# Performance work log

Measured on AMD Instinct MI355X. Metric: run time of the kernel, lower is better.

The kernel has to match this reference:

```python
import jax, jax.numpy as jnp
import numpy as np

B = 32768      # batch
N_IN = 128     # input nodes
L = 8          # topological layers
W = 256        # nodes per layer
K = 16         # fan-in per node


def setup_inputs() -> dict:
    key = jax.random.key(0)
    k_x, k_w, k_b, k_e = jax.random.split(key, 4)
    inputs = jax.random.normal(k_x, (B, N_IN), dtype=jnp.float32)
    # scale weights down so sigmoid isn't saturated with fan-in 16
    weights = jax.random.normal(k_w, (L, W, K), dtype=jnp.float32) * 0.25
    biases = jax.random.normal(k_b, (L, W), dtype=jnp.float32) * 0.1
    # DAG-valid edges: layer l may only gather from the N_IN + l*W already-computed nodes
    ek = jax.random.split(k_e, L)
    edge_idx = jnp.stack([
        jax.random.randint(ek[l], (W, K), 0, N_IN + l * W, dtype=jnp.int32)
        for l in range(L)
    ])  # [L, W, K]
    return {"inputs": inputs, "weights": weights, "biases": biases,
            "edge_idx": edge_idx}


def reference(inputs, weights, biases, edge_idx):
    # values buffer starts as the input-node activations: [B, N_IN]
    vals = inputs
    n_layers = weights.shape[0]
    for l in range(n_layers):
        gathered = vals[:, edge_idx[l]]                      # [B, W, K] per-node gather
        pre = jnp.einsum('bwk,wk->bw', gathered, weights[l]) + biases[l]
        vals = jnp.concatenate([vals, jax.nn.sigmoid(pre)], axis=1)
    # output nodes are the last layer, concatenated in order
    return vals[:, -W:]
```

## Files before the change

### kernel.cpp

```cpp
#include <hip/hip_runtime.h>
#include <hip/hip_bf16.h>
#include <hip/hip_fp16.h>


#define NB   32768
#define NIN  128
#define NL   8
#define NW   256
#define NK   16
#define RPB  16
#define STORED (NIN + (NL - 1) * NW)
#define NPARAM (NL * NW * NK)

typedef __fp16 fp16v2 __attribute__((ext_vector_type(2)));

__device__ __forceinline__ unsigned pk16(float a, float b) {
    fp16v2 p = __builtin_amdgcn_cvt_pkrtz(a, b);
    return __builtin_bit_cast(unsigned, p);
}

__device__ __forceinline__ __half2 as_h2(unsigned u) {
    return __builtin_bit_cast(__half2, u);
}

__device__ __forceinline__ float fast_sigmoid(float x) {
    return __builtin_amdgcn_rcpf(1.0f + __expf(-x));
}

__device__ __forceinline__ void fma_feat(__half2 acc[4], __half2 w2, uint4 p) {
    acc[0] = __hfma2(as_h2(p.x), w2, acc[0]);
    acc[1] = __hfma2(as_h2(p.y), w2, acc[1]);
    acc[2] = __hfma2(as_h2(p.z), w2, acc[2]);
    acc[3] = __hfma2(as_h2(p.w), w2, acc[3]);
}

template <bool PRE>
__global__ __launch_bounds__(256, 2)
void ffn_gather_kernel(const float* __restrict__ inputs,
                       const float* __restrict__ weights,
                       const float* __restrict__ biases,
                       const int*   __restrict__ edge_idx,
                       const int*   __restrict__ idxb,
                       const unsigned* __restrict__ wpk,
                       float* __restrict__ out)
{
    __shared__ uint4 valsA[STORED];
    __shared__ uint4 valsB[STORED];

    const int t = threadIdx.x;
    const long long row0 = (long long)blockIdx.x * RPB;
    const char* vbaseA = (const char*)valsA;
    const char* vbaseB = (const char*)valsB;

    {
        const int f = t & 127;
        const long long r0 = row0 + ((t >> 7) << 3);
        float v[8];
        #pragma unroll
        for (int r = 0; r < 8; ++r) v[r] = inputs[(r0 + r) * NIN + f];
        uint4 p;
        p.x = pk16(v[0], v[1]);
        p.y = pk16(v[2], v[3]);
        p.z = pk16(v[4], v[5]);
        p.w = pk16(v[6], v[7]);
        if (t < NIN) valsA[f] = p; else valsB[f] = p;
    }
    __syncthreads();

    #pragma unroll
    for (int l = 0; l < NL; ++l) {
        const int base = (l * NW + t) * NK;

        const float b = biases[l * NW + t];
        __half2 accA[4], accB[4];
        const __half2 bb = __float2half2_rn(b);
        #pragma unroll
        for (int j = 0; j < 4; ++j) { accA[j] = bb; accB[j] = bb; }

        #pragma unroll
        for (int kk = 0; kk < NK / 4; ++kk) {
            int4 o4;
            __half2 w0, w1, w2, w3;
            if (PRE) {
                o4 = ((const int4*)(idxb + base))[kk];
                uint4 wp = ((const uint4*)(wpk + base))[kk];
                w0 = as_h2(wp.x); w1 = as_h2(wp.y);
                w2 = as_h2(wp.z); w3 = as_h2(wp.w);
            } else {
                int4 i4 = ((const int4*)(edge_idx + base))[kk];
                o4.x = i4.x << 4; o4.y = i4.y << 4;
                o4.z = i4.z << 4; o4.w = i4.w << 4;
                float4 w4 = ((const float4*)(weights + base))[kk];
                w0 = __float2half2_rn(w4.x);
                w1 = __float2half2_rn(w4.y);
                w2 = __float2half2_rn(w4.z);
                w3 = __float2half2_rn(w4.w);
            }
            const uint4 a0 = *(const uint4*)(vbaseA + o4.x);
            const uint4 b0 = *(const uint4*)(vbaseB + o4.x);
            const uint4 a1 = *(const uint4*)(vbaseA + o4.y);
            const uint4 b1 = *(const uint4*)(vbaseB + o4.y);
            const uint4 a2 = *(const uint4*)(vbaseA + o4.z);
            const uint4 b2 = *(const uint4*)(vbaseB + o4.z);
            const uint4 a3 = *(const uint4*)(vbaseA + o4.w);
            const uint4 b3 = *(const uint4*)(vbaseB + o4.w);
            fma_feat(accA, w0, a0);
            fma_feat(accB, w0, b0);
            fma_feat(accA, w1, a1);
            fma_feat(accB, w1, b1);
            fma_feat(accA, w2, a2);
            fma_feat(accB, w2, b2);
            fma_feat(accA, w3, a3);
            fma_feat(accB, w3, b3);
        }

        float sA[8], sB[8];
        #pragma unroll
        for (int j = 0; j < 4; ++j) {
            sA[2 * j + 0] = fast_sigmoid(__low2float(accA[j]));
            sA[2 * j + 1] = fast_sigmoid(__high2float(accA[j]));
            sB[2 * j + 0] = fast_sigmoid(__low2float(accB[j]));
            sB[2 * j + 1] = fast_sigmoid(__high2float(accB[j]));
        }

        if (l < NL - 1) {
            uint4 pA, pB;
            pA.x = pk16(sA[0], sA[1]); pA.y = pk16(sA[2], sA[3]);
            pA.z = pk16(sA[4], sA[5]); pA.w = pk16(sA[6], sA[7]);
            pB.x = pk16(sB[0], sB[1]); pB.y = pk16(sB[2], sB[3]);
            pB.z = pk16(sB[4], sB[5]); pB.w = pk16(sB[6], sB[7]);
            valsA[NIN + l * NW + t] = pA;
            valsB[NIN + l * NW + t] = pB;
            __syncthreads();
        } else {
            #pragma unroll
            for (int r = 0; r < 8; ++r) {
                out[(row0 + r) * NW + t]     = sA[r];
                out[(row0 + 8 + r) * NW + t] = sB[r];
            }
        }
    }
}

__global__ __launch_bounds__(256)
void balance_prepass_kernel(const float* __restrict__ weights,
                            const int* __restrict__ edge_idx,
                            int* __restrict__ idxb,
                            unsigned* __restrict__ wpk)
{
    const int t = blockIdx.x * 256 + threadIdx.x;
    const int lane = threadIdx.x & 63;
    const int base = t * NK;

    int   idxv[NK];
    float wv[NK];
    #pragma unroll
    for (int j = 0; j < NK; ++j) {
        idxv[j] = edge_idx[base + j];
        wv[j]   = weights[base + j];
    }

    unsigned long long cntp = 0;
    #pragma unroll
    for (int j = 0; j < NK; ++j)
        cntp += 1ull << ((idxv[j] & 7) * 8);

    unsigned long long x = cntp;
    x += x << 8;
    x += x << 16;
    x += x << 32;
    unsigned long long cur = x << 8;

    const int rot = (2 * (lane & 7) + ((lane >> 3) & 7)) & 15;
    #pragma unroll
    for (int j = 0; j < NK; ++j) {
        const int g   = idxv[j] & 7;
        const int pos = (int)((cur >> (g * 8)) & 0xFF);
        cur += 1ull << (g * 8);
        const int slot = (pos + rot) & 15;
        idxb[base + slot] = idxv[j] << 4;
        wpk [base + slot] = pk16(wv[j], wv[j]);
    }
}

extern "C" void kernel_launch(void* const* d_in, const int* in_sizes, int n_in,
                              void* d_out, int out_size, void* d_ws, size_t ws_size,
                              hipStream_t stream)
{
    const float* inputs   = (const float*)d_in[0];
    const float* weights  = (const float*)d_in[1];
    const float* biases   = (const float*)d_in[2];
    const int*   edge_idx = (const int*)d_in[3];
    float* out = (float*)d_out;

    dim3 grid(NB / RPB);
    dim3 block(NW);

    const size_t need = (size_t)NPARAM * 4 * 2;
    if (ws_size >= need) {
        int*      idxb = (int*)d_ws;
        unsigned* wpk  = (unsigned*)((char*)d_ws + (size_t)NPARAM * 4);
        balance_prepass_kernel<<<NL * NW / 256, 256, 0, stream>>>(
            weights, edge_idx, idxb, wpk);
        ffn_gather_kernel<true><<<grid, block, 0, stream>>>(
            inputs, weights, biases, edge_idx, idxb, wpk, out);
    } else {
        ffn_gather_kernel<false><<<grid, block, 0, stream>>>(
            inputs, weights, biases, edge_idx, nullptr, nullptr, out);
    }
}
```

Before: 134.1 us.

## Halve rows per block and duplicate LDS values with offset copy for bank balancing

Result: slower. 149.7 us (+11.7%).

```diff
diff --git a/kernel.cpp b/kernel.cpp
--- a/kernel.cpp
+++ b/kernel.cpp
@@ -8,11 +8,14 @@
 #define NL   8
 #define NW   256
 #define NK   16
-#define RPB  16
+#define RPB  8
 #define STORED (NIN + (NL - 1) * NW)
 #define NPARAM (NL * NW * NK)
+#define C1OFF  (STORED * 16)
+#define LDSBYTES (C1OFF + 16 + STORED * 16)
 
 typedef __fp16 fp16v2 __attribute__((ext_vector_type(2)));
+typedef unsigned long long u64;
 
 __device__ __forceinline__ unsigned pk16(float a, float b) {
     fp16v2 p = __builtin_amdgcn_cvt_pkrtz(a, b);
@@ -44,26 +47,22 @@
                        const unsigned* __restrict__ wpk,
                        float* __restrict__ out)
 {
-    __shared__ uint4 valsA[STORED];
-    __shared__ uint4 valsB[STORED];
+    __shared__ __align__(16) char vals[LDSBYTES];
 
     const int t = threadIdx.x;
     const long long row0 = (long long)blockIdx.x * RPB;
-    const char* vbaseA = (const char*)valsA;
-    const char* vbaseB = (const char*)valsB;
 
     {
         const int f = t & 127;
-        const long long r0 = row0 + ((t >> 7) << 3);
         float v[8];
         #pragma unroll
-        for (int r = 0; r < 8; ++r) v[r] = inputs[(r0 + r) * NIN + f];
+        for (int r = 0; r < 8; ++r) v[r] = inputs[(row0 + r) * NIN + f];
         uint4 p;
         p.x = pk16(v[0], v[1]);
         p.y = pk16(v[2], v[3]);
         p.z = pk16(v[4], v[5]);
         p.w = pk16(v[6], v[7]);
-        if (t < NIN) valsA[f] = p; else valsB[f] = p;
+        *(uint4*)(vals + ((t >> 7) ? (C1OFF + 16 + f * 16) : (f * 16))) = p;
     }
     __syncthreads();
 
@@ -72,10 +71,10 @@
         const int base = (l * NW + t) * NK;
 
         const float b = biases[l * NW + t];
-        __half2 accA[4], accB[4];
+        __half2 acc[4];
         const __half2 bb = __float2half2_rn(b);
         #pragma unroll
-        for (int j = 0; j < 4; ++j) { accA[j] = bb; accB[j] = bb; }
+        for (int j = 0; j < 4; ++j) acc[j] = bb;
 
         #pragma unroll
         for (int kk = 0; kk < NK / 4; ++kk) {
@@ -96,48 +95,35 @@
                 w2 = __float2half2_rn(w4.z);
                 w3 = __float2half2_rn(w4.w);
             }
-            const uint4 a0 = *(const uint4*)(vbaseA + o4.x);
-            const uint4 b0 = *(const uint4*)(vbaseB + o4.x);
-            const uint4 a1 = *(const uint4*)(vbaseA + o4.y);
-            const uint4 b1 = *(const uint4*)(vbaseB + o4.y);
-            const uint4 a2 = *(const uint4*)(vbaseA + o4.z);
-            const uint4 b2 = *(const uint4*)(vbaseB + o4.z);
-            const uint4 a3 = *(const uint4*)(vbaseA + o4.w);
-            const uint4 b3 = *(const uint4*)(vbaseB + o4.w);
-            fma_feat(accA, w0, a0);
-            fma_feat(accB, w0, b0);
-            fma_feat(accA, w1, a1);
-            fma_feat(accB, w1, b1);
-            fma_feat(accA, w2, a2);
-            fma_feat(accB, w2, b2);
-            fma_feat(accA, w3, a3);
-            fma_feat(accB, w3, b3);
-        }
-
-        float sA[8], sB[8];
+            const uint4 a0 = *(const uint4*)(vals + o4.x);
+            const uint4 a1 = *(const uint4*)(vals + o4.y);
+            const uint4 a2 = *(const uint4*)(vals + o4.z);
+            const uint4 a3 = *(const uint4*)(vals + o4.w);
+            fma_feat(acc, w0, a0);
+            fma_feat(acc, w1, a1);
+            fma_feat(acc, w2, a2);
+            fma_feat(acc, w3, a3);
+        }
+
+        float s[8];
         #pragma unroll
         for (int j = 0; j < 4; ++j) {
-            sA[2 * j + 0] = fast_sigmoid(__low2float(accA[j]));
-            sA[2 * j + 1] = fast_sigmoid(__high2float(accA[j]));
-            sB[2 * j + 0] = fast_sigmoid(__low2float(accB[j]));
-            sB[2 * j + 1] = fast_sigmoid(__high2float(accB[j]));
+            s[2 * j + 0] = fast_sigmoid(__low2float(acc[j]));
+            s[2 * j + 1] = fast_sigmoid(__high2float(acc[j]));
         }
 
         if (l < NL - 1) {
-            uint4 pA, pB;
-            pA.x = pk16(sA[0], sA[1]); pA.y = pk16(sA[2], sA[3]);
-            pA.z = pk16(sA[4], sA[5]); pA.w = pk16(sA[6], sA[7]);
-            pB.x = pk16(sB[0], sB[1]); pB.y = pk16(sB[2], sB[3]);
-            pB.z = pk16(sB[4], sB[5]); pB.w = pk16(sB[6], sB[7]);
-            valsA[NIN + l * NW + t] = pA;
-            valsB[NIN + l * NW + t] = pB;
+            uint4 p;
+            p.x = pk16(s[0], s[1]); p.y = pk16(s[2], s[3]);
+            p.z = pk16(s[4], s[5]); p.w = pk16(s[6], s[7]);
+            const int F = NIN + l * NW + t;
+            *(uint4*)(vals + F * 16) = p;
+            *(uint4*)(vals + C1OFF + 16 + F * 16) = p;
             __syncthreads();
         } else {
             #pragma unroll
-            for (int r = 0; r < 8; ++r) {
-                out[(row0 + r) * NW + t]     = sA[r];
-                out[(row0 + 8 + r) * NW + t] = sB[r];
-            }
+            for (int r = 0; r < 8; ++r)
+                out[(row0 + r) * NW + t] = s[r];
         }
     }
 }
@@ -149,7 +135,7 @@
                             unsigned* __restrict__ wpk)
 {
     const int t = blockIdx.x * 256 + threadIdx.x;
-    const int lane = threadIdx.x & 63;
+    const int lane = t & 63;
     const int base = t * NK;
 
     int   idxv[NK];
@@ -160,25 +146,58 @@
         wv[j]   = weights[base + j];
     }
 
-    unsigned long long cntp = 0;
+    u64 cntp = 0;
     #pragma unroll
     for (int j = 0; j < NK; ++j)
         cntp += 1ull << ((idxv[j] & 7) * 8);
 
-    unsigned long long x = cntp;
+    u64 s_pk = 0;
+    #pragma unroll
+    for (int it = 0; it < 3; ++it) {
+        #pragma unroll
+        for (int g = 0; g < 8; ++g) {
+            const int gp = (g + 7) & 7;
+            int sp = (int)((s_pk >> (gp * 8)) & 0xFF);
+            int c  = (int)((cntp >> (g * 8)) & 0xFF);
+            int v  = sp + c - 2;
+            v = v < 0 ? 0 : (v > c ? c : v);
+            s_pk = (s_pk & ~(0xFFull << (g * 8))) | ((u64)v << (g * 8));
+        }
+    }
+    const u64 keep_pk = cntp - s_pk;
+
+    u64 used = 0;
+    int fg[NK], sh[NK];
+    #pragma unroll
+    for (int j = 0; j < NK; ++j) {
+        const int g  = idxv[j] & 7;
+        const int u_ = (int)((used >> (g * 8)) & 0xFF);
+        used += 1ull << (g * 8);
+        const int kp = (int)((keep_pk >> (g * 8)) & 0xFF);
+        sh[j] = (u_ >= kp) ? 1 : 0;
+        fg[j] = (g + sh[j]) & 7;
+    }
+
+    u64 fcnt = 0;
+    #pragma unroll
+    for (int j = 0; j < NK; ++j)
+        fcnt += 1ull << (fg[j] * 8);
+
+    u64 x = fcnt;
     x += x << 8;
     x += x << 16;
     x += x << 32;
-    unsigned long long cur = x << 8;
+    u64 cur = x << 8;
 
     const int rot = (2 * (lane & 7) + ((lane >> 3) & 7)) & 15;
     #pragma unroll
     for (int j = 0; j < NK; ++j) {
-        const int g   = idxv[j] & 7;
+        const int g   = fg[j];
         const int pos = (int)((cur >> (g * 8)) & 0xFF);
         cur += 1ull << (g * 8);
         const int slot = (pos + rot) & 15;
-        idxb[base + slot] = idxv[j] << 4;
+        idxb[base + slot] = sh[j] ? (C1OFF + 16 + (idxv[j] << 4))
+                                  : (idxv[j] << 4);
         wpk [base + slot] = pk16(wv[j], wv[j]);
     }
 }
```

## Permute node-to-thread mapping per layer to reduce LDS bank conflicts

Applied to the files above, without the earlier changes.

New measurement: 146.2 us. +9.1%, slower.

```diff
diff --git a/kernel.cpp b/kernel.cpp
--- a/kernel.cpp
+++ b/kernel.cpp
@@ -13,6 +13,7 @@
 #define NPARAM (NL * NW * NK)
 
 typedef __fp16 fp16v2 __attribute__((ext_vector_type(2)));
+typedef unsigned long long u64;
 
 __device__ __forceinline__ unsigned pk16(float a, float b) {
     fp16v2 p = __builtin_amdgcn_cvt_pkrtz(a, b);
@@ -34,7 +35,7 @@
     acc[3] = __hfma2(as_h2(p.w), w2, acc[3]);
 }
 
-template <bool PRE>
+template <bool PRE, bool PERM>
 __global__ __launch_bounds__(256, 2)
 void ffn_gather_kernel(const float* __restrict__ inputs,
                        const float* __restrict__ weights,
@@ -42,6 +43,7 @@
                        const int*   __restrict__ edge_idx,
                        const int*   __restrict__ idxb,
                        const unsigned* __restrict__ wpk,
+                       const int*   __restrict__ punit,
                        float* __restrict__ out)
 {
     __shared__ uint4 valsA[STORED];
@@ -71,7 +73,8 @@
     for (int l = 0; l < NL; ++l) {
         const int base = (l * NW + t) * NK;
 
-        const float b = biases[l * NW + t];
+        const int u = PERM ? punit[l * NW + t] : t;
+        const float b = biases[l * NW + u];
         __half2 accA[4], accB[4];
         const __half2 bb = __float2half2_rn(b);
         #pragma unroll
@@ -135,41 +138,90 @@
         } else {
             #pragma unroll
             for (int r = 0; r < 8; ++r) {
-                out[(row0 + r) * NW + t]     = sA[r];
-                out[(row0 + 8 + r) * NW + t] = sB[r];
+                out[(row0 + r) * NW + u]     = sA[r];
+                out[(row0 + 8 + r) * NW + u] = sB[r];
             }
         }
     }
 }
 
 __global__ __launch_bounds__(256)
-void balance_prepass_kernel(const float* __restrict__ weights,
-                            const int* __restrict__ edge_idx,
-                            int* __restrict__ idxb,
-                            unsigned* __restrict__ wpk)
-{
-    const int t = blockIdx.x * 256 + threadIdx.x;
-    const int lane = threadIdx.x & 63;
-    const int base = t * NK;
+void partition_kernel(const int* __restrict__ edge_idx,
+                      int* __restrict__ t_of,
+                      int* __restrict__ punit)
+{
+    __shared__ int keys[NW];
+    const int l = blockIdx.x;
+    const int u = threadIdx.x;
+
+    u64 c = 0;
+    #pragma unroll
+    for (int j = 0; j < NK; ++j)
+        c += 1ull << ((edge_idx[(l * NW + u) * NK + j] & 7) * 8);
+
+    int best_g = 0, best_v = -1;
+    #pragma unroll
+    for (int g = 0; g < 8; ++g) {
+        const int v = (int)((c >> (g * 8)) & 0xFF);
+        if (v > best_v) { best_v = v; best_g = g; }
+    }
+    keys[u] = best_g * NW + u;
+    __syncthreads();
+
+    const int r = u & 7;
+    const int myk = keys[u];
+    int rank = 0;
+    #pragma unroll
+    for (int j = 0; j < 32; ++j)
+        rank += (keys[8 * j + r] < myk) ? 1 : 0;
+
+    const int o = (rank + 4 * r) & 31;
+    const int t = o * 8 + r;
+    t_of[l * NW + u]  = t;
+    punit[l * NW + t] = u;
+}
+
+template <bool PERM>
+__global__ __launch_bounds__(256)
+void emit_kernel(const float* __restrict__ weights,
+                 const int* __restrict__ edge_idx,
+                 const int* __restrict__ t_of,
+                 const int* __restrict__ punit,
+                 int* __restrict__ idxb,
+                 unsigned* __restrict__ wpk)
+{
+    const int l = blockIdx.x;
+    const int t = threadIdx.x;
+    const int u = PERM ? punit[l * NW + t] : t;
+    const int srcbase = (l * NW + u) * NK;
+    const int dstbase = (l * NW + t) * NK;
+    const int lane = t & 63;
 
     int   idxv[NK];
     float wv[NK];
     #pragma unroll
     for (int j = 0; j < NK; ++j) {
-        idxv[j] = edge_idx[base + j];
-        wv[j]   = weights[base + j];
-    }
-
-    unsigned long long cntp = 0;
+        int ix = edge_idx[srcbase + j];
+        if (PERM && ix >= NIN) {
+            const int f  = ix - NIN;
+            const int ls = f >> 8;
+            const int us = f & 255;
+            ix = NIN + (ls << 8) + t_of[ls * NW + us];
+        }
+        idxv[j] = ix;
+        wv[j]   = weights[srcbase + j];
+    }
+
+    u64 cntp = 0;
     #pragma unroll
     for (int j = 0; j < NK; ++j)
         cntp += 1ull << ((idxv[j] & 7) * 8);
 
-    unsigned long long x = cntp;
+    u64 x = cntp;
     x += x << 8;
     x += x << 16;
     x += x << 32;
-    unsigned long long cur = x << 8;
+    u64 cur = x << 8;
 
     const int rot = (2 * (lane & 7) + ((lane >> 3) & 7)) & 15;
     #pragma unroll
@@ -178,8 +230,8 @@
         const int pos = (int)((cur >> (g * 8)) & 0xFF);
         cur += 1ull << (g * 8);
         const int slot = (pos + rot) & 15;
-        idxb[base + slot] = idxv[j] << 4;
-        wpk [base + slot] = pk16(wv[j], wv[j]);
+        idxb[dstbase + slot] = idxv[j] << 4;
+        wpk [dstbase + slot] = pk16(wv[j], wv[j]);
     }
 }
 
@@ -196,16 +248,31 @@
     dim3 grid(NB / RPB);
     dim3 block(NW);
 
-    const size_t need = (size_t)NPARAM * 4 * 2;
-    if (ws_size >= need) {
+    const size_t sz_idxb  = (size_t)NPARAM * 4;
+    const size_t sz_wpk   = (size_t)NPARAM * 4;
+    const size_t sz_map   = (size_t)NL * NW * 4;
+    const size_t need_basic = sz_idxb + sz_wpk;
+    const size_t need_full  = need_basic + 2 * sz_map;
+
+    if (ws_size >= need_full) {
+        int*      idxb  = (int*)d_ws;
+        unsigned* wpk   = (unsigned*)((char*)d_ws + sz_idxb);
+        int*      t_of  = (int*)((char*)d_ws + need_basic);
+        int*      punit = (int*)((char*)d_ws + need_basic + sz_map);
+        partition_kernel<<<NL, NW, 0, stream>>>(edge_idx, t_of, punit);
+        emit_kernel<true><<<NL, NW, 0, stream>>>(weights, edge_idx,
+                                                 t_of, punit, idxb, wpk);
+        ffn_gather_kernel<true, true><<<grid, block, 0, stream>>>(
+            inputs, weights, biases, edge_idx, idxb, wpk, punit, out);
+    } else if (ws_size >= need_basic) {
         int*      idxb = (int*)d_ws;
-        unsigned* wpk  = (unsigned*)((char*)d_ws + (size_t)NPARAM * 4);
-        balance_prepass_kernel<<<NL * NW / 256, 256, 0, stream>>>(
-            weights, edge_idx, idxb, wpk);
-        ffn_gather_kernel<true><<<grid, block, 0, stream>>>(
-            inputs, weights, biases, edge_idx, idxb, wpk, out);
+        unsigned* wpk  = (unsigned*)((char*)d_ws + sz_idxb);
+        emit_kernel<false><<<NL, NW, 0, stream>>>(weights, edge_idx,
+                                                  nullptr, nullptr, idxb, wpk);
+        ffn_gather_kernel<true, false><<<grid, block, 0, stream>>>(
+            inputs, weights, biases, edge_idx, idxb, wpk, nullptr, out);
     } else {
-        ffn_gather_kernel<false><<<grid, block, 0, stream>>>(
-            inputs, weights, biases, edge_idx, nullptr, nullptr, out);
-    }
-}
+        ffn_gather_kernel<false, false><<<grid, block, 0, stream>>>(
+            inputs, weights, biases, edge_idx, nullptr, nullptr, nullptr, out);
+    }
+}
```

## Pre-pack inputs to fp16 in global memory and gather layer 0 from it

Applied to the files above, without the earlier changes.

Result: slower. 144.1 us (+7.5%).

```diff
diff --git a/kernel.cpp b/kernel.cpp
--- a/kernel.cpp
+++ b/kernel.cpp
@@ -11,8 +11,10 @@
 #define RPB  16
 #define STORED (NIN + (NL - 1) * NW)
 #define NPARAM (NL * NW * NK)
+#define NOCT (NB / 8)
 
 typedef __fp16 fp16v2 __attribute__((ext_vector_type(2)));
+typedef unsigned long long u64;
 
 __device__ __forceinline__ unsigned pk16(float a, float b) {
     fp16v2 p = __builtin_amdgcn_cvt_pkrtz(a, b);
@@ -34,7 +36,7 @@
     acc[3] = __hfma2(as_h2(p.w), w2, acc[3]);
 }
 
-template <bool PRE>
+template <bool PRE, bool G0>
 __global__ __launch_bounds__(256, 2)
 void ffn_gather_kernel(const float* __restrict__ inputs,
                        const float* __restrict__ weights,
@@ -42,6 +44,7 @@
                        const int*   __restrict__ edge_idx,
                        const int*   __restrict__ idxb,
                        const unsigned* __restrict__ wpk,
+                       const uint4* __restrict__ gin,
                        float* __restrict__ out)
 {
     __shared__ uint4 valsA[STORED];
@@ -65,10 +68,63 @@
         p.w = pk16(v[6], v[7]);
         if (t < NIN) valsA[f] = p; else valsB[f] = p;
     }
-    __syncthreads();
-
-    #pragma unroll
-    for (int l = 0; l < NL; ++l) {
+
+    if constexpr (G0) {
+        const char* gA = (const char*)(gin + (size_t)(2 * blockIdx.x)     * NIN);
+        const char* gB = (const char*)(gin + (size_t)(2 * blockIdx.x + 1) * NIN);
+        const int base = t * NK;
+        const float b = biases[t];
+        __half2 accA[4], accB[4];
+        const __half2 bb = __float2half2_rn(b);
+        #pragma unroll
+        for (int j = 0; j < 4; ++j) { accA[j] = bb; accB[j] = bb; }
+
+        #pragma unroll
+        for (int kk = 0; kk < NK / 4; ++kk) {
+            const int4 o4 = ((const int4*)(idxb + base))[kk];
+            const uint4 wp = ((const uint4*)(wpk + base))[kk];
+            const __half2 w0 = as_h2(wp.x), w1 = as_h2(wp.y);
+            const __half2 w2 = as_h2(wp.z), w3 = as_h2(wp.w);
+            const uint4 a0 = *(const uint4*)(gA + o4.x);
+            const uint4 b0 = *(const uint4*)(gB + o4.x);
+            const uint4 a1 = *(const uint4*)(gA + o4.y);
+            const uint4 b1 = *(const uint4*)(gB + o4.y);
+            const uint4 a2 = *(const uint4*)(gA + o4.z);
+            const uint4 b2 = *(const uint4*)(gB + o4.z);
+            const uint4 a3 = *(const uint4*)(gA + o4.w);
+            const uint4 b3 = *(const uint4*)(gB + o4.w);
+            fma_feat(accA, w0, a0);
+            fma_feat(accB, w0, b0);
+            fma_feat(accA, w1, a1);
+            fma_feat(accB, w1, b1);
+            fma_feat(accA, w2, a2);
+            fma_feat(accB, w2, b2);
+            fma_feat(accA, w3, a3);
+            fma_feat(accB, w3, b3);
+        }
+
+        float sA[8], sB[8];
+        #pragma unroll
+        for (int j = 0; j < 4; ++j) {
+            sA[2 * j + 0] = fast_sigmoid(__low2float(accA[j]));
+            sA[2 * j + 1] = fast_sigmoid(__high2float(accA[j]));
+            sB[2 * j + 0] = fast_sigmoid(__low2float(accB[j]));
+            sB[2 * j + 1] = fast_sigmoid(__high2float(accB[j]));
+        }
+        uint4 pA, pB;
+        pA.x = pk16(sA[0], sA[1]); pA.y = pk16(sA[2], sA[3]);
+        pA.z = pk16(sA[4], sA[5]); pA.w = pk16(sA[6], sA[7]);
+        pB.x = pk16(sB[0], sB[1]); pB.y = pk16(sB[2], sB[3]);
+        pB.z = pk16(sB[4], sB[5]); pB.w = pk16(sB[6], sB[7]);
+        valsA[NIN + t] = pA;
+        valsB[NIN + t] = pB;
+        __syncthreads();
+    } else {
+        __syncthreads();
+    }
+
+    #pragma unroll
+    for (int l = G0 ? 1 : 0; l < NL; ++l) {
         const int base = (l * NW + t) * NK;
 
         const float b = biases[l * NW + t];
@@ -143,14 +199,33 @@
 }
 
 __global__ __launch_bounds__(256)
-void balance_prepass_kernel(const float* __restrict__ weights,
-                            const int* __restrict__ edge_idx,
-                            int* __restrict__ idxb,
-                            unsigned* __restrict__ wpk)
+void pack_inputs_kernel(const float* __restrict__ inputs,
+                        uint4* __restrict__ gin)
 {
-    const int t = blockIdx.x * 256 + threadIdx.x;
-    const int lane = threadIdx.x & 63;
-    const int base = t * NK;
+    const int tid = blockIdx.x * 256 + threadIdx.x;
+    const int oc = tid >> 7;
+    const int f  = tid & 127;
+    float v[8];
+    #pragma unroll
+    for (int r = 0; r < 8; ++r)
+        v[r] = inputs[(size_t)(oc * 8 + r) * NIN + f];
+    uint4 p;
+    p.x = pk16(v[0], v[1]);
+    p.y = pk16(v[2], v[3]);
+    p.z = pk16(v[4], v[5]);
+    p.w = pk16(v[6], v[7]);
+    gin[(size_t)oc * NIN + f] = p;
+}
+
+__global__ __launch_bounds__(256)
+void emit_kernel(const float* __restrict__ weights,
+                 const int* __restrict__ edge_idx,
+                 int* __restrict__ idxb,
+                 unsigned* __restrict__ wpk)
+{
+    const int tgid = blockIdx.x * 256 + threadIdx.x;
+    const int lane = tgid & 63;
+    const int base = tgid * NK;
 
     int   idxv[NK];
     float wv[NK];
@@ -160,23 +235,26 @@
         wv[j]   = weights[base + j];
     }
 
-    unsigned long long cntp = 0;
-    #pragma unroll
-    for (int j = 0; j < NK; ++j)
-        cntp += 1ull << ((idxv[j] & 7) * 8);
-
-    unsigned long long x = cntp;
-    x += x << 8;
-    x += x << 16;
-    x += x << 32;
-    unsigned long long cur = x << 8;
+    u64 cA = 0, cB = 0;
+    #pragma unroll
+    for (int j = 0; j < NK; ++j) {
+        const int g = idxv[j] & 15;
+        const u64 inc = 1ull << ((g & 7) * 8);
+        if (g < 8) cA += inc; else cB += inc;
+    }
+    u64 xA = cA; xA += xA << 8; xA += xA << 16; xA += xA << 32;
+    u64 xB = cB; xB += xB << 8; xB += xB << 16; xB += xB << 32;
+    const int totA = (int)((xA >> 56) & 0xFF);
+    u64 curA = xA << 8, curB = xB << 8;
 
     const int rot = (2 * (lane & 7) + ((lane >> 3) & 7)) & 15;
     #pragma unroll
     for (int j = 0; j < NK; ++j) {
-        const int g   = idxv[j] & 7;
-        const int pos = (int)((cur >> (g * 8)) & 0xFF);
-        cur += 1ull << (g * 8);
+        const int g  = idxv[j] & 15;
+        const int gb = (g & 7) * 8;
+        int pos;
+        if (g < 8) { pos = (int)((curA >> gb) & 0xFF);        curA += 1ull << gb; }
+        else       { pos = totA + (int)((curB >> gb) & 0xFF); curB += 1ull << gb; }
         const int slot = (pos + rot) & 15;
         idxb[base + slot] = idxv[j] << 4;
         wpk [base + slot] = pk16(wv[j], wv[j]);
@@ -196,16 +274,27 @@
     dim3 grid(NB / RPB);
     dim3 block(NW);
 
-    const size_t need = (size_t)NPARAM * 4 * 2;
-    if (ws_size >= need) {
+    const size_t sz_tab = (size_t)NPARAM * 4 * 2;
+    const size_t sz_gin = (size_t)NOCT * NIN * 16;
+
+    if (ws_size >= sz_tab + sz_gin) {
         int*      idxb = (int*)d_ws;
         unsigned* wpk  = (unsigned*)((char*)d_ws + (size_t)NPARAM * 4);
-        balance_prepass_kernel<<<NL * NW / 256, 256, 0, stream>>>(
-            weights, edge_idx, idxb, wpk);
-        ffn_gather_kernel<true><<<grid, block, 0, stream>>>(
-            inputs, weights, biases, edge_idx, idxb, wpk, out);
+        uint4*    gin  = (uint4*)((char*)d_ws + sz_tab);
+        pack_inputs_kernel<<<NOCT * NIN / 256, 256, 0, stream>>>(inputs, gin);
+        emit_kernel<<<NL * NW / 256, 256, 0, stream>>>(weights, edge_idx,
+                                                       idxb, wpk);
+        ffn_gather_kernel<true, true><<<grid, block, 0, stream>>>(
+            inputs, weights, biases, edge_idx, idxb, wpk, gin, out);
+    } else if (ws_size >= sz_tab) {
+        int*      idxb = (int*)d_ws;
+        unsigned* wpk  = (unsigned*)((char*)d_ws + (size_t)NPARAM * 4);
+        emit_kernel<<<NL * NW / 256, 256, 0, stream>>>(weights, edge_idx,
+                                                       idxb, wpk);
+        ffn_gather_kernel<true, false><<<grid, block, 0, stream>>>(
+            inputs, weights, biases, edge_idx, idxb, wpk, nullptr, out);
     } else {
-        ffn_gather_kernel<false><<<grid, block, 0, stream>>>(
-            inputs, weights, biases, edge_idx, nullptr, nullptr, out);
-    }
-}
+        ffn_gather_kernel<false, false><<<grid, block, 0, stream>>>(
+            inputs, weights, biases, edge_idx, nullptr, nullptr, nullptr, out);
+    }
+}
```
